# Kernel tuning notes

Measured on AMD Instinct MI355X. Metric: run time of the kernel, lower is better.

Reference implementation:

```python
import itertools
import jax, jax.numpy as jnp
import numpy as np

NUM_GROUPS = 2  # num_squeeze_group
LN_EPS = 1e-6


def setup_inputs() -> dict:
    key = jax.random.key(0)
    ks = jax.random.split(key, 8)
    B, F, D = 1024, 32, 64
    P = F * (F - 1) // 2  # 496 pairs
    OUT = 512
    g = NUM_GROUPS
    red = max(1, F * g * 2 // 4)  # reduction_ratio = 4 -> 32
    emb_size = F * D
    return {
        "x": jax.random.normal(ks[0], (B, F, D), jnp.float32),
        "W1": jax.random.normal(ks[1], (F * 2 * g, red), jnp.float32) * (1.0 / np.sqrt(F * 2 * g)),
        "b1": jnp.zeros((red,), jnp.float32),
        "W2": jax.random.normal(ks[2], (red, emb_size), jnp.float32) * (1.0 / np.sqrt(red)),
        "b2": jnp.zeros((emb_size,), jnp.float32),
        "ln_scale": jnp.ones((emb_size,), jnp.float32),
        "ln_bias": jnp.zeros((emb_size,), jnp.float32),
        "Wp": jax.random.normal(ks[3], (P, D, D), jnp.float32) * (1.0 / np.sqrt(D)),
        "bp": jnp.zeros((P, D), jnp.float32),
        "Wo": jax.random.normal(ks[4], (P, OUT), jnp.float32) * (1.0 / np.sqrt(P)),
        "bo": jnp.zeros((OUT,), jnp.float32),
    }


def _pair_indices(F):
    pairs = np.array(list(itertools.combinations(range(F), 2)), dtype=np.int32)
    return pairs[:, 0], pairs[:, 1]


def reference(x, W1, b1, W2, b2, ln_scale, ln_bias, Wp, bp, Wo, bo):
    B, F, D = x.shape
    g = NUM_GROUPS

    # ---- SENet ----
    xg = x.reshape(B, F, g, D // g)
    # per-field [max(g), mean(g)], concatenated over fields -> [B, F*2g]
    z = jnp.concatenate([xg.max(axis=-1), xg.mean(axis=-1)], axis=-1).reshape(B, F * 2 * g)
    a1 = jax.nn.relu(z @ W1 + b1)            # [B, red]
    weights = a1 @ W2 + b2                   # [B, F*D]
    flat = x.reshape(B, F * D)
    senet = flat * weights + flat            # skip connection
    # layer norm over last axis
    mu = senet.mean(axis=-1, keepdims=True)
    var = senet.var(axis=-1, keepdims=True)
    senet = (senet - mu) * jax.lax.rsqrt(var + LN_EPS) * ln_scale + ln_bias

    # ---- BiLinear ('interaction', use_plus=True) ----
    i_idx, j_idx = _pair_indices(F)
    xi = x[:, i_idx, :]                      # [B, P, D]
    xj = x[:, j_idx, :]                      # [B, P, D]
    proj = jnp.einsum('bpd,pde->bpe', xi, Wp) + bp  # per-pair Dense(D->D)
    dots = jnp.sum(proj * xj, axis=-1)       # [B, P] batched dot (bi-linear+)
    bilinear = dots @ Wo + bo                # [B, OUT]

    return jnp.concatenate([senet, bilinear], axis=-1)
```

## Files before the change

kernel.cpp:

```cpp
#include <hip/hip_runtime.h>
#include <hip/hip_bf16.h>

#define F_FEAT 32
#define D_DIM 64
#define B_SZ 1024
#define EMB 2048
#define P_PAIRS 496
#define KPAD 512
#define OUT_N 512
#define OUT_STRIDE 2560
#define LN_EPS 1e-6f

typedef __attribute__((ext_vector_type(8))) short bf16x8;
typedef __attribute__((ext_vector_type(4))) float f32x4;

__device__ inline ushort f2bf(float f) {
    union { float f; unsigned u; } a; a.f = f;
    unsigned u = a.u;
    unsigned r = (u + 0x7FFFu + ((u >> 16) & 1u)) >> 16;
    return (ushort)r;
}
__device__ inline float bf2f(ushort u) {
    union { unsigned u; float f; } a; a.u = ((unsigned)u) << 16;
    return a.f;
}

__global__ __launch_bounds__(256) void k_prep(
        const float* __restrict__ Wp, ushort* __restrict__ Wpt,
        const float* __restrict__ Wo, ushort* __restrict__ Wot,
        ushort* __restrict__ db) {
    __shared__ float tile[64][65];
    int t = threadIdx.x;
    int blk = blockIdx.x;

    if (blk < 496) {
        int p = blk;
        const float* src = Wp + (size_t)p * 4096;
        ushort* dst = Wpt + (size_t)p * 4096;
#pragma unroll
        for (int it = 0; it < 4; ++it) {
            int d = it * 16 + (t >> 4);
            int e4 = (t & 15) * 4;
            float4 v = *reinterpret_cast<const float4*>(src + d * 64 + e4);
            tile[d][e4] = v.x; tile[d][e4 + 1] = v.y; tile[d][e4 + 2] = v.z; tile[d][e4 + 3] = v.w;
        }
        __syncthreads();
#pragma unroll
        for (int it = 0; it < 4; ++it) {
            int e = it * 16 + (t >> 4);
            int d4 = (t & 15) * 4;
            ushort4 o;
            o.x = f2bf(tile[d4][e]);     o.y = f2bf(tile[d4 + 1][e]);
            o.z = f2bf(tile[d4 + 2][e]); o.w = f2bf(tile[d4 + 3][e]);
            *reinterpret_cast<ushort4*>(dst + e * 64 + d4) = o;
        }
    } else if (blk < 560) {
        int bidx = blk - 496;
        int k0 = (bidx & 7) * 64;
        int n0 = (bidx >> 3) * 64;
#pragma unroll
        for (int it = 0; it < 4; ++it) {
            int kr = it * 16 + (t >> 4);
            int nc = (t & 15) * 4;
            int k = k0 + kr;
            float4 v = {0.f, 0.f, 0.f, 0.f};
            if (k < P_PAIRS) v = *reinterpret_cast<const float4*>(Wo + (size_t)k * OUT_N + n0 + nc);
            tile[kr][nc] = v.x; tile[kr][nc + 1] = v.y; tile[kr][nc + 2] = v.z; tile[kr][nc + 3] = v.w;
        }
        __syncthreads();
#pragma unroll
        for (int it = 0; it < 4; ++it) {
            int nr = it * 16 + (t >> 4);
            int kc = (t & 15) * 4;
            ushort4 o;
            o.x = f2bf(tile[kc][nr]);     o.y = f2bf(tile[kc + 1][nr]);
            o.z = f2bf(tile[kc + 2][nr]); o.w = f2bf(tile[kc + 3][nr]);
            *reinterpret_cast<ushort4*>(Wot + (size_t)(n0 + nr) * KPAD + k0 + kc) = o;
        }
    } else {
        int tid = (blk - 560) * 256 + t;
        if (tid < B_SZ) {
            bf16x8 z = {0, 0, 0, 0, 0, 0, 0, 0};
            ushort* dstp = db + (size_t)tid * KPAD + P_PAIRS;
            *reinterpret_cast<bf16x8*>(dstp) = z;
            *reinterpret_cast<bf16x8*>(dstp + 8) = z;
        }
    }
}

__global__ __launch_bounds__(512) void k_senet(
        const float* __restrict__ x, ushort* __restrict__ xb,
        const float* __restrict__ W1, const float* __restrict__ b1,
        const float* __restrict__ W2, const float* __restrict__ b2,
        const float* __restrict__ ln_s, const float* __restrict__ ln_b,
        float* __restrict__ out) {
    __shared__ float xs[4][EMB];
    __shared__ float zs[4][128];
    __shared__ float a1s[4][32];
    __shared__ float red[2][4][8];
    __shared__ float mlpred[2][128];
    int t = threadIdx.x;
    int b0 = blockIdx.x * 4;

    for (int r = 0; r < 4; ++r) {
        const float4* src = reinterpret_cast<const float4*>(x + (size_t)(b0 + r) * EMB);
        float4 v = src[t];
        reinterpret_cast<float4*>(&xs[r][0])[t] = v;
        ushort4 o;
        o.x = f2bf(v.x); o.y = f2bf(v.y); o.z = f2bf(v.z); o.w = f2bf(v.w);
        *reinterpret_cast<ushort4*>(xb + (size_t)(b0 + r) * EMB + t * 4) = o;
    }
    __syncthreads();

    {
        int g2 = t >> 1, sub = t & 1;
        int r = g2 >> 6, fg = g2 & 63, f = fg >> 1, gg = fg & 1;
        const float* base = &xs[r][f * 64 + gg * 32 + sub * 16];
        float mx = -INFINITY, sm = 0.f;
#pragma unroll
        for (int q = 0; q < 16; ++q) {
            float v = base[(q + t) & 15];
            mx = fmaxf(mx, v); sm += v;
        }
        float mx2 = __shfl_xor(mx, 1);
        float sm2 = __shfl_xor(sm, 1);
        mx = fmaxf(mx, mx2); sm += sm2;
        if (sub == 0) {
            zs[r][f * 4 + gg]     = mx;
            zs[r][f * 4 + 2 + gg] = sm * (1.f / 32.f);
        }
    }
    __syncthreads();

    if (t < 256) {
        int chunk = t >> 7, c = t & 127;
        int r = c >> 5, cc = c & 31;
        float acc = 0.f;
        int k0 = chunk * 64;
#pragma unroll
        for (int k = 0; k < 64; ++k) acc += zs[r][k0 + k] * W1[(k0 + k) * 32 + cc];
        mlpred[chunk][c] = acc;
    }
    __syncthreads();
    if (t < 128) {
        int r = t >> 5, cc = t & 31;
        a1s[r][cc] = fmaxf(mlpred[0][t] + mlpred[1][t] + b1[cc], 0.f);
    }
    __syncthreads();

    float acc[4][4];
#pragma unroll
    for (int r = 0; r < 4; ++r)
#pragma unroll
        for (int u = 0; u < 4; ++u) acc[r][u] = 0.f;

    for (int k = 0; k < 32; ++k) {
        float a0 = a1s[0][k], a1v = a1s[1][k], a2 = a1s[2][k], a3 = a1s[3][k];
#pragma unroll
        for (int u = 0; u < 4; ++u) {
            float wv = W2[k * EMB + t + 512 * u];
            acc[0][u] += a0 * wv; acc[1][u] += a1v * wv;
            acc[2][u] += a2 * wv; acc[3][u] += a3 * wv;
        }
    }
    float ssum[4], ssq[4];
#pragma unroll
    for (int r = 0; r < 4; ++r) { ssum[r] = 0.f; ssq[r] = 0.f; }
#pragma unroll
    for (int r = 0; r < 4; ++r) {
#pragma unroll
        for (int u = 0; u < 4; ++u) {
            int e = t + 512 * u;
            float w = acc[r][u] + b2[e];
            float s = xs[r][e] * (w + 1.0f);
            xs[r][e] = s;
            ssum[r] += s; ssq[r] += s * s;
        }
    }
    int lane = t & 63, w = t >> 6;
#pragma unroll
    for (int r = 0; r < 4; ++r) {
        float a = ssum[r], q = ssq[r];
        for (int off = 32; off; off >>= 1) { a += __shfl_down(a, off); q += __shfl_down(q, off); }
        if (lane == 0) { red[0][r][w] = a; red[1][r][w] = q; }
    }
    __syncthreads();
    float mu[4], rs[4];
#pragma unroll
    for (int r = 0; r < 4; ++r) {
        float a = 0.f, q = 0.f;
#pragma unroll
        for (int i = 0; i < 8; ++i) { a += red[0][r][i]; q += red[1][r][i]; }
        mu[r] = a * (1.f / 2048.f);
        float var = q * (1.f / 2048.f) - mu[r] * mu[r];
        rs[r] = rsqrtf(var + LN_EPS);
    }
#pragma unroll
    for (int r = 0; r < 4; ++r) {
#pragma unroll
        for (int u = 0; u < 4; ++u) {
            int e = t + 512 * u;
            float s = xs[r][e];
            out[(size_t)(b0 + r) * OUT_STRIDE + e] = (s - mu[r]) * rs[r] * ln_s[e] + ln_b[e];
        }
    }
}

__global__ __launch_bounds__(256) void k_dots(
        const ushort* __restrict__ xb, const ushort* __restrict__ Wpt,
        const float* __restrict__ bp, ushort* __restrict__ db) {
    int p = blockIdx.x >> 1;
    int h = blockIdx.x & 1;
    int i = 0, rem = p;
    while (rem >= F_FEAT - 1 - i) { rem -= F_FEAT - 1 - i; ++i; }
    int j = i + 1 + rem;

    int wave = threadIdx.x >> 6, lane = threadIdx.x & 63;
    int row = lane & 15, kg = lane >> 4;

    bf16x8 wfr[4][2];
#pragma unroll
    for (int nt = 0; nt < 4; ++nt)
#pragma unroll
        for (int ks = 0; ks < 2; ++ks)
            wfr[nt][ks] = *reinterpret_cast<const bf16x8*>(
                Wpt + (size_t)p * 4096 + (nt * 16 + row) * 64 + ks * 32 + kg * 8);

    f32x4 bb[4];
#pragma unroll
    for (int nt = 0; nt < 4; ++nt)
        bb[nt] = *reinterpret_cast<const f32x4*>(bp + p * 64 + nt * 16 + kg * 4);

    const ushort* xi_base = xb + (size_t)row * EMB + i * 64 + kg * 8;
    const ushort* xj_base = xb + (size_t)row * EMB + j * 64 + kg * 4;

    bf16x8 xifr[2][2];
    ushort4 xjw[2][4];

    auto loadit = [&](int it, int buf) {
        size_t boff = (size_t)(h * 512 + (wave * 8 + it) * 16) * EMB;
#pragma unroll
        for (int ks = 0; ks < 2; ++ks)
            xifr[buf][ks] = *reinterpret_cast<const bf16x8*>(xi_base + boff + ks * 32);
#pragma unroll
        for (int nt = 0; nt < 4; ++nt)
            xjw[buf][nt] = *reinterpret_cast<const ushort4*>(xj_base + boff + nt * 16);
    };

    loadit(0, 0);
#pragma unroll
    for (int it = 0; it < 8; ++it) {
        int cur = it & 1;
        if (it < 7) loadit(it + 1, cur ^ 1);

        f32x4 acc[4];
#pragma unroll
        for (int nt = 0; nt < 4; ++nt) {
            acc[nt] = bb[nt];
            acc[nt] = __builtin_amdgcn_mfma_f32_16x16x32_bf16(wfr[nt][0], xifr[cur][0], acc[nt], 0, 0, 0);
            acc[nt] = __builtin_amdgcn_mfma_f32_16x16x32_bf16(wfr[nt][1], xifr[cur][1], acc[nt], 0, 0, 0);
        }

        float v = 0.f;
#pragma unroll
        for (int nt = 0; nt < 4; ++nt) {
            v += acc[nt][0] * bf2f(xjw[cur][nt].x);
            v += acc[nt][1] * bf2f(xjw[cur][nt].y);
            v += acc[nt][2] * bf2f(xjw[cur][nt].z);
            v += acc[nt][3] * bf2f(xjw[cur][nt].w);
        }
        v += __shfl_xor(v, 16);
        v += __shfl_xor(v, 32);
        if (lane < 16) {
            int b0 = h * 512 + (wave * 8 + it) * 16;
            db[(size_t)(b0 + lane) * KPAD + p] = f2bf(v);
        }
    }
}

__global__ __launch_bounds__(256) void k_bilin2(
        const ushort* __restrict__ db, const ushort* __restrict__ Wot,
        const float* __restrict__ bo, float* __restrict__ out) {
    int mt  = blockIdx.x >> 4;
    int nt0 = blockIdx.x & 15;
    int wave = threadIdx.x >> 6, lane = threadIdx.x & 63;
    int row = lane & 15, kg = lane >> 4;
    int m0 = mt * 64 + wave * 16;
    int n0 = nt0 * 32;

    f32x4 acc0 = {0.f, 0.f, 0.f, 0.f};
    f32x4 acc1 = {0.f, 0.f, 0.f, 0.f};
    const ushort* arow  = db  + (size_t)(m0 + row) * KPAD + kg * 8;
    const ushort* brow0 = Wot + (size_t)(n0 + row) * KPAD + kg * 8;
    const ushort* brow1 = brow0 + 16 * KPAD;
#pragma unroll
    for (int ks = 0; ks < 16; ++ks) {
        bf16x8 a  = *reinterpret_cast<const bf16x8*>(arow  + ks * 32);
        bf16x8 b0 = *reinterpret_cast<const bf16x8*>(brow0 + ks * 32);
        bf16x8 b1 = *reinterpret_cast<const bf16x8*>(brow1 + ks * 32);
        acc0 = __builtin_amdgcn_mfma_f32_16x16x32_bf16(a, b0, acc0, 0, 0, 0);
        acc1 = __builtin_amdgcn_mfma_f32_16x16x32_bf16(a, b1, acc1, 0, 0, 0);
    }
    int col = row;
    float bo0 = bo[n0 + col], bo1 = bo[n0 + 16 + col];
#pragma unroll
    for (int r = 0; r < 4; ++r) {
        size_t orow = (size_t)(m0 + kg * 4 + r) * OUT_STRIDE + 2048 + n0;
        out[orow + col]      = acc0[r] + bo0;
        out[orow + 16 + col] = acc1[r] + bo1;
    }
}

extern "C" void kernel_launch(void* const* d_in, const int* in_sizes, int n_in,
                              void* d_out, int out_size, void* d_ws, size_t ws_size,
                              hipStream_t stream) {
    const float* x    = (const float*)d_in[0];
    const float* W1   = (const float*)d_in[1];
    const float* b1   = (const float*)d_in[2];
    const float* W2   = (const float*)d_in[3];
    const float* b2   = (const float*)d_in[4];
    const float* ln_s = (const float*)d_in[5];
    const float* ln_b = (const float*)d_in[6];
    const float* Wp   = (const float*)d_in[7];
    const float* bp   = (const float*)d_in[8];
    const float* Wo   = (const float*)d_in[9];
    const float* bo   = (const float*)d_in[10];
    float* out = (float*)d_out;

    ushort* xb   = (ushort*)d_ws;
    ushort* wpt  = (ushort*)((char*)d_ws + 4194304);
    ushort* db   = (ushort*)((char*)d_ws + 4194304 + 4063232);
    ushort* wot  = (ushort*)((char*)d_ws + 4194304 + 4063232 + 1048576);

    k_prep<<<568, 256, 0, stream>>>(Wp, wpt, Wo, wot, db);
    k_senet<<<B_SZ / 4, 512, 0, stream>>>(x, xb, W1, b1, W2, b2, ln_s, ln_b, out);
    k_dots<<<P_PAIRS * 2, 256, 0, stream>>>(xb, wpt, bp, db);
    k_bilin2<<<256, 256, 0, stream>>>(db, wot, bo, out);
}
```

Before: 57.30 us.

## Fuse prep and SENet kernels; split dots and bilinear grids finer

Merges the weight transpose/convert prep kernel and the SENet kernel into one launch of 512-thread blocks, with a shared-memory union covering both roles. This removes one launch and lets the two independent pieces of work run at the same time. k_dots now uses four batch quarters per pair instead of two, and k_bilin2 uses smaller 32x32 tiles with each wave splitting K into two accumulators, so both launch more blocks. The risk is fewer resident blocks, since every front block reserves the larger shared allocation. The finer grids also mean more redundant weight loads and shorter pipelines per block.

```diff
diff --git a/kernel.cpp b/kernel.cpp
--- a/kernel.cpp
+++ b/kernel.cpp
@@ -25,60 +25,181 @@
     return a.f;
 }
 
-__global__ __launch_bounds__(256) void k_prep(
+__global__ __launch_bounds__(512) void k_front(
+        const float* __restrict__ x, ushort* __restrict__ xb,
+        const float* __restrict__ W1, const float* __restrict__ b1,
+        const float* __restrict__ W2, const float* __restrict__ b2,
+        const float* __restrict__ ln_s, const float* __restrict__ ln_b,
         const float* __restrict__ Wp, ushort* __restrict__ Wpt,
         const float* __restrict__ Wo, ushort* __restrict__ Wot,
-        ushort* __restrict__ db) {
-    __shared__ float tile[64][65];
+        ushort* __restrict__ db, float* __restrict__ out) {
+    __shared__ union {
+        struct {
+            float xs[4][EMB];
+            float zs[4][128];
+            float a1s[4][32];
+            float red[2][4][8];
+            float mlpred[2][128];
+        } sn;
+        float tile[64][65];
+    } sm;
     int t = threadIdx.x;
     int blk = blockIdx.x;
 
-    if (blk < 496) {
-        int p = blk;
+    if (blk < 256) {
+        int b0 = blk * 4;
+
+        for (int r = 0; r < 4; ++r) {
+            const float4* src = reinterpret_cast<const float4*>(x + (size_t)(b0 + r) * EMB);
+            float4 v = src[t];
+            reinterpret_cast<float4*>(&sm.sn.xs[r][0])[t] = v;
+            ushort4 o;
+            o.x = f2bf(v.x); o.y = f2bf(v.y); o.z = f2bf(v.z); o.w = f2bf(v.w);
+            *reinterpret_cast<ushort4*>(xb + (size_t)(b0 + r) * EMB + t * 4) = o;
+        }
+        __syncthreads();
+
+        {
+            int g2 = t >> 1, sub = t & 1;
+            int r = g2 >> 6, fg = g2 & 63, f = fg >> 1, gg = fg & 1;
+            const float* base = &sm.sn.xs[r][f * 64 + gg * 32 + sub * 16];
+            float mx = -INFINITY, smv = 0.f;
+#pragma unroll
+            for (int q = 0; q < 16; ++q) {
+                float v = base[(q + t) & 15];
+                mx = fmaxf(mx, v); smv += v;
+            }
+            float mx2 = __shfl_xor(mx, 1);
+            float sm2 = __shfl_xor(smv, 1);
+            mx = fmaxf(mx, mx2); smv += sm2;
+            if (sub == 0) {
+                sm.sn.zs[r][f * 4 + gg]     = mx;
+                sm.sn.zs[r][f * 4 + 2 + gg] = smv * (1.f / 32.f);
+            }
+        }
+        __syncthreads();
+
+        if (t < 256) {
+            int chunk = t >> 7, c = t & 127;
+            int r = c >> 5, cc = c & 31;
+            float acc = 0.f;
+            int k0 = chunk * 64;
+#pragma unroll
+            for (int k = 0; k < 64; ++k) acc += sm.sn.zs[r][k0 + k] * W1[(k0 + k) * 32 + cc];
+            sm.sn.mlpred[chunk][c] = acc;
+        }
+        __syncthreads();
+        if (t < 128) {
+            int r = t >> 5, cc = t & 31;
+            sm.sn.a1s[r][cc] = fmaxf(sm.sn.mlpred[0][t] + sm.sn.mlpred[1][t] + b1[cc], 0.f);
+        }
+        __syncthreads();
+
+        float acc[4][4];
+#pragma unroll
+        for (int r = 0; r < 4; ++r)
+#pragma unroll
+            for (int u = 0; u < 4; ++u) acc[r][u] = 0.f;
+
+        for (int k = 0; k < 32; ++k) {
+            float a0 = sm.sn.a1s[0][k], a1v = sm.sn.a1s[1][k];
+            float a2 = sm.sn.a1s[2][k], a3 = sm.sn.a1s[3][k];
+#pragma unroll
+            for (int u = 0; u < 4; ++u) {
+                float wv = W2[k * EMB + t + 512 * u];
+                acc[0][u] += a0 * wv; acc[1][u] += a1v * wv;
+                acc[2][u] += a2 * wv; acc[3][u] += a3 * wv;
+            }
+        }
+        float ssum[4], ssq[4];
+#pragma unroll
+        for (int r = 0; r < 4; ++r) { ssum[r] = 0.f; ssq[r] = 0.f; }
+#pragma unroll
+        for (int r = 0; r < 4; ++r) {
+#pragma unroll
+            for (int u = 0; u < 4; ++u) {
+                int e = t + 512 * u;
+                float w = acc[r][u] + b2[e];
+                float s = sm.sn.xs[r][e] * (w + 1.0f);
+                sm.sn.xs[r][e] = s;
+                ssum[r] += s; ssq[r] += s * s;
+            }
+        }
+        int lane = t & 63, w = t >> 6;
+#pragma unroll
+        for (int r = 0; r < 4; ++r) {
+            float a = ssum[r], q = ssq[r];
+            for (int off = 32; off; off >>= 1) { a += __shfl_down(a, off); q += __shfl_down(q, off); }
+            if (lane == 0) { sm.sn.red[0][r][w] = a; sm.sn.red[1][r][w] = q; }
+        }
+        __syncthreads();
+        float mu[4], rs[4];
+#pragma unroll
+        for (int r = 0; r < 4; ++r) {
+            float a = 0.f, q = 0.f;
+#pragma unroll
+            for (int i = 0; i < 8; ++i) { a += sm.sn.red[0][r][i]; q += sm.sn.red[1][r][i]; }
+            mu[r] = a * (1.f / 2048.f);
+            float var = q * (1.f / 2048.f) - mu[r] * mu[r];
+            rs[r] = rsqrtf(var + LN_EPS);
+        }
+#pragma unroll
+        for (int r = 0; r < 4; ++r) {
+#pragma unroll
+            for (int u = 0; u < 4; ++u) {
+                int e = t + 512 * u;
+                float s = sm.sn.xs[r][e];
+                out[(size_t)(b0 + r) * OUT_STRIDE + e] = (s - mu[r]) * rs[r] * ln_s[e] + ln_b[e];
+            }
+        }
+    } else if (blk < 752) {
+        int p = blk - 256;
         const float* src = Wp + (size_t)p * 4096;
         ushort* dst = Wpt + (size_t)p * 4096;
 #pragma unroll
-        for (int it = 0; it < 4; ++it) {
-            int d = it * 16 + (t >> 4);
+        for (int it = 0; it < 2; ++it) {
+            int d = it * 32 + (t >> 4);
             int e4 = (t & 15) * 4;
             float4 v = *reinterpret_cast<const float4*>(src + d * 64 + e4);
-            tile[d][e4] = v.x; tile[d][e4 + 1] = v.y; tile[d][e4 + 2] = v.z; tile[d][e4 + 3] = v.w;
-        }
-        __syncthreads();
-#pragma unroll
-        for (int it = 0; it < 4; ++it) {
-            int e = it * 16 + (t >> 4);
+            sm.tile[d][e4] = v.x; sm.tile[d][e4 + 1] = v.y;
+            sm.tile[d][e4 + 2] = v.z; sm.tile[d][e4 + 3] = v.w;
+        }
+        __syncthreads();
+#pragma unroll
+        for (int it = 0; it < 2; ++it) {
+            int e = it * 32 + (t >> 4);
             int d4 = (t & 15) * 4;
             ushort4 o;
-            o.x = f2bf(tile[d4][e]);     o.y = f2bf(tile[d4 + 1][e]);
-            o.z = f2bf(tile[d4 + 2][e]); o.w = f2bf(tile[d4 + 3][e]);
+            o.x = f2bf(sm.tile[d4][e]);     o.y = f2bf(sm.tile[d4 + 1][e]);
+            o.z = f2bf(sm.tile[d4 + 2][e]); o.w = f2bf(sm.tile[d4 + 3][e]);
             *reinterpret_cast<ushort4*>(dst + e * 64 + d4) = o;
         }
-    } else if (blk < 560) {
-        int bidx = blk - 496;
+    } else if (blk < 816) {
+        int bidx = blk - 752;
         int k0 = (bidx & 7) * 64;
         int n0 = (bidx >> 3) * 64;
 #pragma unroll
-        for (int it = 0; it < 4; ++it) {
-            int kr = it * 16 + (t >> 4);
+        for (int it = 0; it < 2; ++it) {
+            int kr = it * 32 + (t >> 4);
             int nc = (t & 15) * 4;
             int k = k0 + kr;
             float4 v = {0.f, 0.f, 0.f, 0.f};
             if (k < P_PAIRS) v = *reinterpret_cast<const float4*>(Wo + (size_t)k * OUT_N + n0 + nc);
-            tile[kr][nc] = v.x; tile[kr][nc + 1] = v.y; tile[kr][nc + 2] = v.z; tile[kr][nc + 3] = v.w;
-        }
-        __syncthreads();
-#pragma unroll
-        for (int it = 0; it < 4; ++it) {
-            int nr = it * 16 + (t >> 4);
+            sm.tile[kr][nc] = v.x; sm.tile[kr][nc + 1] = v.y;
+            sm.tile[kr][nc + 2] = v.z; sm.tile[kr][nc + 3] = v.w;
+        }
+        __syncthreads();
+#pragma unroll
+        for (int it = 0; it < 2; ++it) {
+            int nr = it * 32 + (t >> 4);
             int kc = (t & 15) * 4;
             ushort4 o;
-            o.x = f2bf(tile[kc][nr]);     o.y = f2bf(tile[kc + 1][nr]);
-            o.z = f2bf(tile[kc + 2][nr]); o.w = f2bf(tile[kc + 3][nr]);
+            o.x = f2bf(sm.tile[kc][nr]);     o.y = f2bf(sm.tile[kc + 1][nr]);
+            o.z = f2bf(sm.tile[kc + 2][nr]); o.w = f2bf(sm.tile[kc + 3][nr]);
             *reinterpret_cast<ushort4*>(Wot + (size_t)(n0 + nr) * KPAD + k0 + kc) = o;
         }
     } else {
-        int tid = (blk - 560) * 256 + t;
+        int tid = (blk - 816) * 512 + t;
         if (tid < B_SZ) {
             bf16x8 z = {0, 0, 0, 0, 0, 0, 0, 0};
             ushort* dstp = db + (size_t)tid * KPAD + P_PAIRS;
@@ -88,129 +209,11 @@
     }
 }
 
-__global__ __launch_bounds__(512) void k_senet(
-        const float* __restrict__ x, ushort* __restrict__ xb,
-        const float* __restrict__ W1, const float* __restrict__ b1,
-        const float* __restrict__ W2, const float* __restrict__ b2,
-        const float* __restrict__ ln_s, const float* __restrict__ ln_b,
-        float* __restrict__ out) {
-    __shared__ float xs[4][EMB];
-    __shared__ float zs[4][128];
-    __shared__ float a1s[4][32];
-    __shared__ float red[2][4][8];
-    __shared__ float mlpred[2][128];
-    int t = threadIdx.x;
-    int b0 = blockIdx.x * 4;
-
-    for (int r = 0; r < 4; ++r) {
-        const float4* src = reinterpret_cast<const float4*>(x + (size_t)(b0 + r) * EMB);
-        float4 v = src[t];
-        reinterpret_cast<float4*>(&xs[r][0])[t] = v;
-        ushort4 o;
-        o.x = f2bf(v.x); o.y = f2bf(v.y); o.z = f2bf(v.z); o.w = f2bf(v.w);
-        *reinterpret_cast<ushort4*>(xb + (size_t)(b0 + r) * EMB + t * 4) = o;
-    }
-    __syncthreads();
-
-    {
-        int g2 = t >> 1, sub = t & 1;
-        int r = g2 >> 6, fg = g2 & 63, f = fg >> 1, gg = fg & 1;
-        const float* base = &xs[r][f * 64 + gg * 32 + sub * 16];
-        float mx = -INFINITY, sm = 0.f;
-#pragma unroll
-        for (int q = 0; q < 16; ++q) {
-            float v = base[(q + t) & 15];
-            mx = fmaxf(mx, v); sm += v;
-        }
-        float mx2 = __shfl_xor(mx, 1);
-        float sm2 = __shfl_xor(sm, 1);
-        mx = fmaxf(mx, mx2); sm += sm2;
-        if (sub == 0) {
-            zs[r][f * 4 + gg]     = mx;
-            zs[r][f * 4 + 2 + gg] = sm * (1.f / 32.f);
-        }
-    }
-    __syncthreads();
-
-    if (t < 256) {
-        int chunk = t >> 7, c = t & 127;
-        int r = c >> 5, cc = c & 31;
-        float acc = 0.f;
-        int k0 = chunk * 64;
-#pragma unroll
-        for (int k = 0; k < 64; ++k) acc += zs[r][k0 + k] * W1[(k0 + k) * 32 + cc];
-        mlpred[chunk][c] = acc;
-    }
-    __syncthreads();
-    if (t < 128) {
-        int r = t >> 5, cc = t & 31;
-        a1s[r][cc] = fmaxf(mlpred[0][t] + mlpred[1][t] + b1[cc], 0.f);
-    }
-    __syncthreads();
-
-    float acc[4][4];
-#pragma unroll
-    for (int r = 0; r < 4; ++r)
-#pragma unroll
-        for (int u = 0; u < 4; ++u) acc[r][u] = 0.f;
-
-    for (int k = 0; k < 32; ++k) {
-        float a0 = a1s[0][k], a1v = a1s[1][k], a2 = a1s[2][k], a3 = a1s[3][k];
-#pragma unroll
-        for (int u = 0; u < 4; ++u) {
-            float wv = W2[k * EMB + t + 512 * u];
-            acc[0][u] += a0 * wv; acc[1][u] += a1v * wv;
-            acc[2][u] += a2 * wv; acc[3][u] += a3 * wv;
-        }
-    }
-    float ssum[4], ssq[4];
-#pragma unroll
-    for (int r = 0; r < 4; ++r) { ssum[r] = 0.f; ssq[r] = 0.f; }
-#pragma unroll
-    for (int r = 0; r < 4; ++r) {
-#pragma unroll
-        for (int u = 0; u < 4; ++u) {
-            int e = t + 512 * u;
-            float w = acc[r][u] + b2[e];
-            float s = xs[r][e] * (w + 1.0f);
-            xs[r][e] = s;
-            ssum[r] += s; ssq[r] += s * s;
-        }
-    }
-    int lane = t & 63, w = t >> 6;
-#pragma unroll
-    for (int r = 0; r < 4; ++r) {
-        float a = ssum[r], q = ssq[r];
-        for (int off = 32; off; off >>= 1) { a += __shfl_down(a, off); q += __shfl_down(q, off); }
-        if (lane == 0) { red[0][r][w] = a; red[1][r][w] = q; }
-    }
-    __syncthreads();
-    float mu[4], rs[4];
-#pragma unroll
-    for (int r = 0; r < 4; ++r) {
-        float a = 0.f, q = 0.f;
-#pragma unroll
-        for (int i = 0; i < 8; ++i) { a += red[0][r][i]; q += red[1][r][i]; }
-        mu[r] = a * (1.f / 2048.f);
-        float var = q * (1.f / 2048.f) - mu[r] * mu[r];
-        rs[r] = rsqrtf(var + LN_EPS);
-    }
-#pragma unroll
-    for (int r = 0; r < 4; ++r) {
-#pragma unroll
-        for (int u = 0; u < 4; ++u) {
-            int e = t + 512 * u;
-            float s = xs[r][e];
-            out[(size_t)(b0 + r) * OUT_STRIDE + e] = (s - mu[r]) * rs[r] * ln_s[e] + ln_b[e];
-        }
-    }
-}
-
 __global__ __launch_bounds__(256) void k_dots(
         const ushort* __restrict__ xb, const ushort* __restrict__ Wpt,
         const float* __restrict__ bp, ushort* __restrict__ db) {
-    int p = blockIdx.x >> 1;
-    int h = blockIdx.x & 1;
+    int p = blockIdx.x >> 2;
+    int q = blockIdx.x & 3;
     int i = 0, rem = p;
     while (rem >= F_FEAT - 1 - i) { rem -= F_FEAT - 1 - i; ++i; }
     int j = i + 1 + rem;
@@ -238,7 +241,7 @@
     ushort4 xjw[2][4];
 
     auto loadit = [&](int it, int buf) {
-        size_t boff = (size_t)(h * 512 + (wave * 8 + it) * 16) * EMB;
+        size_t boff = (size_t)(q * 256 + (wave * 4 + it) * 16) * EMB;
 #pragma unroll
         for (int ks = 0; ks < 2; ++ks)
             xifr[buf][ks] = *reinterpret_cast<const bf16x8*>(xi_base + boff + ks * 32);
@@ -249,9 +252,9 @@
 
     loadit(0, 0);
 #pragma unroll
-    for (int it = 0; it < 8; ++it) {
+    for (int it = 0; it < 4; ++it) {
         int cur = it & 1;
-        if (it < 7) loadit(it + 1, cur ^ 1);
+        if (it < 3) loadit(it + 1, cur ^ 1);
 
         f32x4 acc[4];
 #pragma unroll
@@ -272,7 +275,7 @@
         v += __shfl_xor(v, 16);
         v += __shfl_xor(v, 32);
         if (lane < 16) {
-            int b0 = h * 512 + (wave * 8 + it) * 16;
+            int b0 = q * 256 + (wave * 4 + it) * 16;
             db[(size_t)(b0 + lane) * KPAD + p] = f2bf(v);
         }
     }
@@ -284,30 +287,30 @@
     int mt  = blockIdx.x >> 4;
     int nt0 = blockIdx.x & 15;
     int wave = threadIdx.x >> 6, lane = threadIdx.x & 63;
+    int wm = wave & 1, wn = wave >> 1;
     int row = lane & 15, kg = lane >> 4;
-    int m0 = mt * 64 + wave * 16;
-    int n0 = nt0 * 32;
+    int m0 = mt * 32 + wm * 16;
+    int n0 = nt0 * 32 + wn * 16;
 
     f32x4 acc0 = {0.f, 0.f, 0.f, 0.f};
     f32x4 acc1 = {0.f, 0.f, 0.f, 0.f};
-    const ushort* arow  = db  + (size_t)(m0 + row) * KPAD + kg * 8;
-    const ushort* brow0 = Wot + (size_t)(n0 + row) * KPAD + kg * 8;
-    const ushort* brow1 = brow0 + 16 * KPAD;
-#pragma unroll
-    for (int ks = 0; ks < 16; ++ks) {
-        bf16x8 a  = *reinterpret_cast<const bf16x8*>(arow  + ks * 32);
-        bf16x8 b0 = *reinterpret_cast<const bf16x8*>(brow0 + ks * 32);
-        bf16x8 b1 = *reinterpret_cast<const bf16x8*>(brow1 + ks * 32);
-        acc0 = __builtin_amdgcn_mfma_f32_16x16x32_bf16(a, b0, acc0, 0, 0, 0);
-        acc1 = __builtin_amdgcn_mfma_f32_16x16x32_bf16(a, b1, acc1, 0, 0, 0);
+    const ushort* arow = db  + (size_t)(m0 + row) * KPAD + kg * 8;
+    const ushort* brow = Wot + (size_t)(n0 + row) * KPAD + kg * 8;
+#pragma unroll
+    for (int ks = 0; ks < 16; ks += 2) {
+        bf16x8 a0 = *reinterpret_cast<const bf16x8*>(arow + ks * 32);
+        bf16x8 b0 = *reinterpret_cast<const bf16x8*>(brow + ks * 32);
+        bf16x8 a1 = *reinterpret_cast<const bf16x8*>(arow + (ks + 1) * 32);
+        bf16x8 b1 = *reinterpret_cast<const bf16x8*>(brow + (ks + 1) * 32);
+        acc0 = __builtin_amdgcn_mfma_f32_16x16x32_bf16(a0, b0, acc0, 0, 0, 0);
+        acc1 = __builtin_amdgcn_mfma_f32_16x16x32_bf16(a1, b1, acc1, 0, 0, 0);
     }
     int col = row;
-    float bo0 = bo[n0 + col], bo1 = bo[n0 + 16 + col];
+    float bov = bo[n0 + col];
 #pragma unroll
     for (int r = 0; r < 4; ++r) {
         size_t orow = (size_t)(m0 + kg * 4 + r) * OUT_STRIDE + 2048 + n0;
-        out[orow + col]      = acc0[r] + bo0;
-        out[orow + 16 + col] = acc1[r] + bo1;
+        out[orow + col] = acc0[r] + acc1[r] + bov;
     }
 }
 
@@ -332,8 +335,8 @@
     ushort* db   = (ushort*)((char*)d_ws + 4194304 + 4063232);
     ushort* wot  = (ushort*)((char*)d_ws + 4194304 + 4063232 + 1048576);
 
-    k_prep<<<568, 256, 0, stream>>>(Wp, wpt, Wo, wot, db);
-    k_senet<<<B_SZ / 4, 512, 0, stream>>>(x, xb, W1, b1, W2, b2, ln_s, ln_b, out);
-    k_dots<<<P_PAIRS * 2, 256, 0, stream>>>(xb, wpt, bp, db);
-    k_bilin2<<<256, 256, 0, stream>>>(db, wot, bo, out);
-}
+    k_front<<<818, 512, 0, stream>>>(x, xb, W1, b1, W2, b2, ln_s, ln_b,
+                                     Wp, wpt, Wo, wot, db, out);
+    k_dots<<<P_PAIRS * 4, 256, 0, stream>>>(xb, wpt, bp, db);
+    k_bilin2<<<512, 256, 0, stream>>>(db, wot, bo, out);
+}
```

After: 57.61 us. No clear change (+0.5%).
